# Performance work log

Measured on AMD Instinct MI355X. Metric: run time of the kernel, lower is better.

The kernel has to match this reference:

```python
import jax, jax.numpy as jnp
import numpy as np

LMAX = 6; MMAX = 2
C = 128          # num_channels
H = 8            # num_heads
ALPHA = 32       # attn_alpha_channels
VAL = 16         # attn_value_channels (H*VAL == C)
HID = 64         # attn_hidden_channels
FFN = 128        # ffn_hidden_channels
NL = 4           # num_layers
CUTOFF = 12.0; NRBF = 600
AVG_DEG = 23.395238876342773
AVG_NODES = 77.81317
EPS = 1e-16

def _maps():
    idx, ls = [], []
    for l in range(LMAX + 1):
        mm = min(l, MMAX)
        for m in range(-mm, mm + 1):
            idx.append(l * l + l + m); ls.append(l)
    return np.array(idx), np.array(ls)
_M2F_np, _LOF_np = _maps()
M2F = jnp.asarray(_M2F_np)   # [KM] full-coefficient index of each m-restricted coeff
LOF = jnp.asarray(_LOF_np)   # [KM] degree l of each m-restricted coeff
KM = int(_M2F_np.shape[0])   # 29 for lmax=6, mmax=2
KF = (LMAX + 1) ** 2         # 49

def _rbf(d):
    # GaussianSmearing(0, cutoff, NRBF, width_scalar=2.0)
    off = jnp.linspace(0.0, CUTOFF, NRBF)
    coeff = -0.5 / (2.0 * (off[1] - off[0])) ** 2
    return jnp.exp(coeff * (d[:, None] - off) ** 2)

def _envelope(d):
    # PolynomialEnvelope, exponent p=5
    x = d / CUTOFF
    env = 1.0 - 21.0 * x ** 5 + 35.0 * x ** 6 - 15.0 * x ** 7
    return jnp.where(x < 1.0, env, 0.0)

def _rms(x, g):
    # merge-norm over channel dim with learned per-channel scale
    return x * jax.lax.rsqrt(jnp.mean(x * x, axis=-1, keepdims=True) + 1e-6) * g

def _forward(atomic_numbers, edge_index, edge_distance, emb,
             We0, be0, We1, be1, Weproj, gamma1, gamma2,
             Wr0, Wr1, Wrl, Wmsg, Wap, wa, Wg, Wv, Wo,
             Wf1, Wfg, Wf2, Wh1, Wh2):
    N = atomic_numbers.shape[0]
    src, tgt = edge_index[0], edge_index[1]
    rbf = _rbf(edge_distance)            # [E, NRBF]
    env = _envelope(edge_distance)       # [E]
    # node init: atom embedding on the l=0 component
    x = jnp.zeros((N, KF, C), rbf.dtype).at[:, 0, :].set(emb[atomic_numbers])
    # edge-degree embedding: radial MLP -> per-edge coeffs -> scatter to targets
    h = jax.nn.silu(rbf @ We0 + be0)
    h = jax.nn.silu(h @ We1 + be1)
    deg = (h @ Weproj).reshape(-1, KM, C)              # [E, KM, C]
    x = x.at[tgt[:, None], M2F[None, :], :].add(deg / AVG_DEG)
    for i in range(NL):
        # ---- equivariant graph attention ----
        y = _rms(x, gamma1[i])
        ym = y[:, M2F, :]                               # [N, KM, C] m-restricted
        m = jnp.concatenate([ym[src], ym[tgt]], axis=-1)  # [E, KM, 2C]
        m = jnp.einsum('ekc,ch->ekh', m, Wmsg[i])       # [E, KM, HID]
        # radial function, shared across m within each l (use_rad_l_parametrization)
        rad = jax.nn.silu(jax.nn.silu(rbf @ Wr0[i]) @ Wr1[i])
        radl = rad @ Wrl[i]                             # [E, LMAX+1]
        m = m * radl[:, LOF][..., None]
        # attention logits from invariant (l=0) part
        a = jax.nn.silu(m[:, 0, :] @ Wap[i]).reshape(-1, H, ALPHA)
        logits = jnp.einsum('eha,ha->eh', a, wa[i])     # [E, H]
        segmax = jnp.full((N, H), -jnp.inf, logits.dtype).at[tgt].max(logits)
        ex = env[:, None] * jnp.exp(logits - segmax[tgt])  # envelope-masked softmax
        den = jax.ops.segment_sum(ex, tgt, num_segments=N)
        attn = ex / (den[tgt] + EPS)                    # [E, H]
        # SwiGLU-gated equivariant values
        g = jax.nn.silu(m[:, 0, :] @ Wg[i])             # [E, H*VAL]
        v = jnp.einsum('ekh,hv->ekv', m, Wv[i]) * g[:, None, :]
        v = v.reshape(-1, KM, H, VAL) * attn[:, None, :, None]
        agg = jax.ops.segment_sum(v.reshape(-1, KM, H * VAL), tgt, num_segments=N)
        out = jnp.einsum('nkv,vc->nkc', agg, Wo[i])     # [N, KM, C]
        x = x.at[:, M2F, :].add(out)
        # ---- feed-forward (grid-MLP style SwiGLU) ----
        y = _rms(x, gamma2[i])
        gf = jax.nn.silu(y[:, 0, :] @ Wfg[i])           # [N, FFN]
        hf = jnp.einsum('nkc,cf->nkf', y, Wf1[i]) * gf[:, None, :]
        x = x + jnp.einsum('nkf,fc->nkc', hf, Wf2[i])
    # energy head on invariant part, sum-aggregated over nodes
    s = jax.nn.silu(x[:, 0, :] @ Wh1) @ Wh2             # [N, 1]
    return (jnp.sum(s) / AVG_NODES).reshape(1)

def setup_inputs() -> dict:
    key = jax.random.key(0)
    ks = jax.random.split(key, 24)
    N, E = 6000, 120000
    def rn(k, shape, scale=0.05):
        return jax.random.normal(k, shape, dtype=jnp.float32) * scale
    inp = {}
    inp['atomic_numbers'] = jax.random.randint(ks[0], (N,), 0, 128)
    inp['edge_index'] = jax.random.randint(ks[1], (2, E), 0, N)
    inp['edge_distance'] = jax.random.uniform(ks[2], (E,), minval=0.5, maxval=CUTOFF, dtype=jnp.float32)
    inp['emb'] = rn(ks[3], (128, C), 1.0)
    inp['We0'] = rn(ks[4], (NRBF, 128)); inp['be0'] = jnp.zeros((128,), jnp.float32)
    inp['We1'] = rn(ks[5], (128, 128)); inp['be1'] = jnp.zeros((128,), jnp.float32)
    inp['Weproj'] = rn(ks[6], (128, KM * C))
    inp['gamma1'] = jnp.ones((NL, C), jnp.float32)
    inp['gamma2'] = jnp.ones((NL, C), jnp.float32)
    inp['Wr0'] = rn(ks[7], (NL, NRBF, 128))
    inp['Wr1'] = rn(ks[8], (NL, 128, 128))
    inp['Wrl'] = rn(ks[9], (NL, 128, LMAX + 1), 0.1)
    inp['Wmsg'] = rn(ks[10], (NL, 2 * C, HID))
    inp['Wap'] = rn(ks[11], (NL, HID, H * ALPHA))
    inp['wa'] = rn(ks[12], (NL, H, ALPHA))
    inp['Wg'] = rn(ks[13], (NL, HID, H * VAL))
    inp['Wv'] = rn(ks[14], (NL, HID, H * VAL))
    inp['Wo'] = rn(ks[15], (NL, H * VAL, C))
    inp['Wf1'] = rn(ks[16], (NL, C, FFN))
    inp['Wfg'] = rn(ks[17], (NL, C, FFN))
    inp['Wf2'] = rn(ks[18], (NL, FFN, C))
    inp['Wh1'] = rn(ks[19], (C, C))
    inp['Wh2'] = rn(ks[20], (C, 1))
    return inp

def reference(atomic_numbers, edge_index, edge_distance, emb,
              We0, be0, We1, be1, Weproj, gamma1, gamma2,
              Wr0, Wr1, Wrl, Wmsg, Wap, wa, Wg, Wv, Wo,
              Wf1, Wfg, Wf2, Wh1, Wh2):
    return _forward(atomic_numbers, edge_index, edge_distance, emb,
                    We0, be0, We1, be1, Weproj, gamma1, gamma2,
                    Wr0, Wr1, Wrl, Wmsg, Wap, wa, Wg, Wv, Wo,
                    Wf1, Wfg, Wf2, Wh1, Wh2)
```

## Files before the change

kernel.cpp:

```cpp
#include <hip/hip_runtime.h>

#define KM 29
#define GTAB 2048

typedef __bf16 bf16_t;
typedef __bf16 bf16x8 __attribute__((ext_vector_type(8)));
typedef __bf16 bf16x4 __attribute__((ext_vector_type(4)));
typedef __bf16 bf16x2 __attribute__((ext_vector_type(2)));
typedef float  f32x4  __attribute__((ext_vector_type(4)));
typedef float  f32x2  __attribute__((ext_vector_type(2)));

__device__ __forceinline__ float silu_f(float x){ return x / (1.0f + __expf(-x)); }

__device__ __forceinline__ float wave_reduce_sum(float v){
  #pragma unroll
  for (int s = 1; s < 64; s <<= 1) v += __shfl_xor(v, s);
  return v;
}

__device__ __forceinline__ constexpr int LOF2(int k){
  return (k<1)?0 : (k<4)?1 : (k<9)?2 : (k<14)?3 : (k<19)?4 : (k<24)?5 : 6;
}

__device__ __forceinline__ f32x4 mfma16(bf16x8 a, bf16x8 b, f32x4 c){
  return __builtin_amdgcn_mfma_f32_16x16x32_bf16(a, b, c, 0, 0, 0);
}

__device__ __forceinline__ float env_f(float d){
  float xx = d*(1.0f/12.0f);
  float x2 = xx*xx, x4 = x2*x2, x5 = x4*xx;
  float env = 1.0f - 21.0f*x5 + 35.0f*x5*xx - 15.0f*x5*x2;
  return (xx < 1.0f) ? env : 0.0f;
}

__global__ void k_count(const int* __restrict__ EI, int* __restrict__ cnt, int E){
  int e = blockIdx.x*256 + threadIdx.x;
  if (e < E) atomicAdd(&cnt[EI[E+e]], 1);
}

__global__ __launch_bounds__(1024) void k_scan(int* __restrict__ cnt, int* __restrict__ rowptr, int N){
  __shared__ int ts[1024];
  int t = threadIdx.x;
  int base = t*8;
  int loc[8]; int sum = 0;
  #pragma unroll
  for (int u = 0; u < 8; u++){ int idx = base+u; int v = (idx < N) ? cnt[idx] : 0; loc[u] = sum; sum += v; }
  ts[t] = sum; __syncthreads();
  for (int off = 1; off < 1024; off <<= 1){
    int v = (t >= off) ? ts[t-off] : 0;
    __syncthreads();
    ts[t] += v;
    __syncthreads();
  }
  int excl = ts[t] - sum;
  #pragma unroll
  for (int u = 0; u < 8; u++){
    int idx = base+u;
    if (idx < N){ int r = excl + loc[u]; rowptr[idx] = r; cnt[idx] = r; }
  }
  if (t == 1023) rowptr[N] = ts[1023];
}

__global__ void k_fill(const int* __restrict__ EI, int* __restrict__ cur, int* __restrict__ order, int E){
  int e = blockIdx.x*256 + threadIdx.x;
  if (e < E){ int pos = atomicAdd(&cur[EI[E+e]], 1); order[pos] = e; }
}

__global__ void k_sort(const int* __restrict__ rowptr, int* __restrict__ order, int N){
  int n = blockIdx.x*256 + threadIdx.x;
  if (n >= N) return;
  int rp = rowptr[n], re = rowptr[n+1];
  for (int a = rp+1; a < re; a++){
    int key = order[a]; int b = a-1;
    while (b >= rp && order[b] > key){ order[b+1] = order[b]; b--; }
    order[b+1] = key;
  }
}

__global__ void k_tr(const float* __restrict__ src, bf16_t* __restrict__ dst,
                     int L, int R, int C, int Lstr){
  int idx = blockIdx.x*256 + threadIdx.x;
  int total = L*R*C;
  if (idx >= total) return;
  int l = idx / (R*C); int rem = idx - l*(R*C);
  int r = rem / C; int c = rem - r*C;
  dst[((size_t)l*C + c)*R + r] = (bf16_t)src[(size_t)l*Lstr + (size_t)r*C + c];
}

__global__ void k_tr2(const float* __restrict__ src, bf16_t* __restrict__ dst){
  int idx = blockIdx.x*256 + threadIdx.x;
  if (idx >= 4*128*128) return;
  int l = idx >> 14; int j = (idx >> 7) & 127; int c = idx & 127;
  float v = (j < 64) ? src[(size_t)l*16384 + c*64 + j]
                     : src[(size_t)l*16384 + 8192 + c*64 + (j-64)];
  dst[idx] = (bf16_t)v;
}

__global__ __launch_bounds__(256) void k_tab_embed(
    const float* __restrict__ We0, const float* __restrict__ be0,
    const float* __restrict__ We1, const float* __restrict__ be1,
    const float* __restrict__ Wr0, const float* __restrict__ Wr1, const float* __restrict__ Wrl,
    float* __restrict__ h2tab, float* __restrict__ radtab)
{
  __shared__ float sb[4][640];
  const int wid = threadIdx.x >> 6, lane = threadIdx.x & 63;
  const int e = blockIdx.x*4 + wid;
  if (e >= GTAB) return;
  const float d = e * (12.0f/(GTAB-1));
  const float DLT = 12.0f/599.0f;
  const float CO  = -0.5f/((2.0f*DLT)*(2.0f*DLT));
  int jc = (int)(d/DLT + 0.5f);
  int j0 = jc - 16; if (j0 < 0) j0 = 0; if (j0 > 600-32) j0 = 600-32;
  float diff = d - (float)(j0+lane)*DLT;
  float gval = __expf(CO*diff*diff);
  float p[10];
  #pragma unroll
  for (int u = 0; u < 10; u++) p[u] = 0.f;
  const int c2 = 2*lane;
  for (int jj = 0; jj < 32; jj++){
    float gj = __shfl(gval, jj);
    int row = j0 + jj;
    const float2 w0 = *(const float2*)(We0 + row*128 + c2);
    p[0] += gj*w0.x; p[1] += gj*w0.y;
    #pragma unroll
    for (int i = 0; i < 4; i++){
      const float2 wr = *(const float2*)(Wr0 + ((size_t)i*600 + row)*128 + c2);
      p[2+2*i] += gj*wr.x; p[3+2*i] += gj*wr.y;
    }
  }
  sb[wid][c2]   = silu_f(p[0] + be0[c2]);
  sb[wid][c2+1] = silu_f(p[1] + be0[c2+1]);
  #pragma unroll
  for (int i = 0; i < 4; i++){
    sb[wid][128 + 128*i + c2]   = silu_f(p[2+2*i]);
    sb[wid][128 + 128*i + c2+1] = silu_f(p[3+2*i]);
  }
  float a0 = 0.f, a1 = 0.f;
  for (int c = 0; c < 128; c++){
    float hv = sb[wid][c];
    const float2 w = *(const float2*)(We1 + c*128 + c2);
    a0 += hv*w.x; a1 += hv*w.y;
  }
  a0 = silu_f(a0 + be1[c2]); a1 = silu_f(a1 + be1[c2+1]);
  h2tab[(size_t)e*128 + c2]     = a0;
  h2tab[(size_t)e*128 + c2 + 1] = a1;
  #pragma unroll
  for (int i = 0; i < 4; i++){
    float r0 = 0.f, r1 = 0.f;
    const float* W1 = Wr1 + (size_t)i*128*128;
    for (int c = 0; c < 128; c++){
      float rv = sb[wid][128 + 128*i + c];
      const float2 w = *(const float2*)(W1 + c*128 + c2);
      r0 += rv*w.x; r1 += rv*w.y;
    }
    r0 = silu_f(r0); r1 = silu_f(r1);
    const float* Wl = Wrl + (size_t)i*128*7;
    float pl[7];
    #pragma unroll
    for (int l = 0; l < 7; l++) pl[l] = r0*Wl[c2*7+l] + r1*Wl[(c2+1)*7+l];
    #pragma unroll
// ... 232 lines not shown
    #pragma unroll
    for (int r = 0; r < 4; r++){
      int e = eb + lg*4 + r;
      if (e < E) gate16[(size_t)e*128 + col] = (bf16_t)silu_f(accG[u][r]);
    }
  }
  #pragma unroll
  for (int hpair = 0; hpair < 2; hpair++){
    int c0 = 64*wid + hpair*32 + l15;
    float w0 = wav[c0], w1 = wav[c0+16];
    float s[4];
    #pragma unroll
    for (int r = 0; r < 4; r++)
      s[r] = silu_f(accA[2*hpair][r])*w0 + silu_f(accA[2*hpair+1][r])*w1;
    #pragma unroll
    for (int r = 0; r < 4; r++){
      s[r] += __shfl_xor(s[r], 1);
      s[r] += __shfl_xor(s[r], 2);
      s[r] += __shfl_xor(s[r], 4);
      s[r] += __shfl_xor(s[r], 8);
    }
    if (l15 == 0){
      #pragma unroll
      for (int r = 0; r < 4; r++){
        int e = eb + lg*4 + r;
        if (e < E) expat[(size_t)e*8 + 2*wid + hpair] = envs[lg*4 + r] * __expf(s[r]);
      }
    }
  }
}

#define FMA_DW(dw, kb) { \
  f32x2 lo_ = __builtin_amdgcn_cvt_pk_f32_fp8((dw), false); \
  f32x2 hi_ = __builtin_amdgcn_cvt_pk_f32_fp8((dw), true); \
  acc[(kb)]   += lo_.x * rw[LOF2((kb))]; \
  acc[(kb)+1] += lo_.y * rw[LOF2((kb)+1)]; \
  acc[(kb)+2] += hi_.x * rw[LOF2((kb)+2)]; \
  acc[(kb)+3] += hi_.y * rw[LOF2((kb)+3)]; }

__global__ __launch_bounds__(512, 4) void k_gather(
    const int* __restrict__ EI, const int* __restrict__ rowptr, const int* __restrict__ order,
    const unsigned char* __restrict__ PV8, const unsigned char* __restrict__ QV8,
    const bf16_t* __restrict__ gate16, const float* __restrict__ expat,
    const float* __restrict__ radl,
    bf16_t* __restrict__ agg)
{
  __shared__ bf16_t mA[32*136];
  __shared__ bf16_t mB[32*136];
  __shared__ float at8[512];
  __shared__ float rl7[512];
  __shared__ int   esb[64], srcs[64];
  __shared__ float denl[32];

  int n = blockIdx.x, t = threadIdx.x;
  int rp = rowptr[n], deg = rowptr[n+1] - rp;
  if (deg == 0){
    for (int idx = t; idx < 3712; idx += 512) agg[(size_t)n*3712 + idx] = (bf16_t)0.f;
    return;
  }
  int eg = t >> 7, hv = t & 127, h = hv >> 4;
  float acc[32];
  #pragma unroll
  for (int j = 0; j < 32; j++) acc[j] = 0.f;
  float S[7];
  #pragma unroll
  for (int l = 0; l < 7; l++) S[l] = 0.f;
  float dpart = 0.f;
  for (int base = 0; base < deg; base += 64){
    int ne = min(64, deg - base);
    if (base > 0) __syncthreads();
    if (t < ne){ int e = order[rp + base + t]; esb[t] = e; srcs[t] = EI[e]; }
    __syncthreads();
    if (t < ne*8){
      int i = t >> 3, q = t & 7;
      int e = esb[i];
      at8[t] = expat[(size_t)e*8 + q];
      if (q < 7) rl7[t] = radl[(size_t)e*7 + q];
    }
    __syncthreads();
    uint4 A0 = {0,0,0,0}, A1 = {0,0,0,0}, B0 = {0,0,0,0}, B1 = {0,0,0,0};
    float gA = 0.f, gB = 0.f;
    int i = eg;
    if (i < ne){
      const uint4* p = (const uint4*)(PV8 + (size_t)srcs[i]*4096 + hv*32);
      A0 = p[0]; A1 = p[1];
      gA = (float)gate16[(size_t)esb[i]*128 + hv];
    }
    if (i + 4 < ne){
      const uint4* p = (const uint4*)(PV8 + (size_t)srcs[i+4]*4096 + hv*32);
      B0 = p[0]; B1 = p[1];
      gB = (float)gate16[(size_t)esb[i+4]*128 + hv];
    }
    while (i < ne){
      int i2 = i + 8;
      uint4 C0 = {0,0,0,0}, C1 = {0,0,0,0}; float gC = 0.f;
      if (i2 < ne){
        const uint4* p = (const uint4*)(PV8 + (size_t)srcs[i2]*4096 + hv*32);
        C0 = p[0]; C1 = p[1];
        gC = (float)gate16[(size_t)esb[i2]*128 + hv];
      }
      float ae = at8[i*8 + h];
      dpart += ae;
      float w = gA * ae;
      float rw[7];
      #pragma unroll
      for (int l = 0; l < 7; l++){ rw[l] = rl7[i*8 + l]*w; S[l] += rw[l]; }
      FMA_DW(A0.x, 0)  FMA_DW(A0.y, 4)  FMA_DW(A0.z, 8)  FMA_DW(A0.w, 12)
      FMA_DW(A1.x, 16) FMA_DW(A1.y, 20) FMA_DW(A1.z, 24) FMA_DW(A1.w, 28)
      A0 = B0; A1 = B1; gA = gB;
      B0 = C0; B1 = C1; gB = gC;
      i += 4;
    }
  }
  {
    const unsigned char* qvp = QV8 + (size_t)n*4096 + hv*32;
    uint4 q0 = *(const uint4*)qvp;
    uint4 q1 = *(const uint4*)(qvp + 16);
    float rw[7];
    #pragma unroll
    for (int l = 0; l < 7; l++) rw[l] = S[l];
    FMA_DW(q0.x, 0)  FMA_DW(q0.y, 4)  FMA_DW(q0.z, 8)  FMA_DW(q0.w, 12)
    FMA_DW(q1.x, 16) FMA_DW(q1.y, 20) FMA_DW(q1.z, 24) FMA_DW(q1.w, 28)
  }
  if ((hv & 15) == 0) denl[eg*8 + h] = dpart;
  __syncthreads();
  {
    float dsum = denl[h] + denl[8 + h] + denl[16 + h] + denl[24 + h];
    float inv = 1.0f/(dsum + 1e-30f);
    #pragma unroll
    for (int j = 0; j < 32; j++) acc[j] *= inv;
  }
  if (eg == 0){
    #pragma unroll
    for (int j = 0; j < 32; j++) mA[j*136 + hv] = (bf16_t)acc[j];
  } else if (eg == 1){
    #pragma unroll
    for (int j = 0; j < 32; j++) mB[j*136 + hv] = (bf16_t)acc[j];
  }
  __syncthreads();
  if (eg == 2){
    #pragma unroll
    for (int j = 0; j < 32; j++) mA[j*136 + hv] = (bf16_t)((float)mA[j*136 + hv] + acc[j]);
  } else if (eg == 3){
    #pragma unroll
    for (int j = 0; j < 32; j++) mB[j*136 + hv] = (bf16_t)((float)mB[j*136 + hv] + acc[j]);
  }
  __syncthreads();
  for (int idx = t; idx < 3712; idx += 512){
    int k = idx >> 7, c = idx & 127;
    agg[(size_t)n*3712 + idx] = (bf16_t)((float)mA[k*136 + c] + (float)mB[k*136 + c]);
  }
}

__global__ __launch_bounds__(512, 4) void k_xupdate(
    const bf16_t* __restrict__ agg,
    const float* __restrict__ gamma1, const float* __restrict__ gamma2,
    const float* __restrict__ Wfg,
    const bf16_t* __restrict__ Wf1T, const bf16_t* __restrict__ Wf2T,
    const bf16_t* __restrict__ WoT, const bf16_t* __restrict__ WmsgCT, const bf16_t* __restrict__ WvT,
    bf16_t* __restrict__ Xb, int layer,
    unsigned char* __restrict__ PV8o, unsigned char* __restrict__ QV8o,
    float* __restrict__ P0o, float* __restrict__ Q0o, int do_tail, int N)
{
  __shared__ float  xs[3712];
  __shared__ bf16_t ysag[32*136];
  __shared__ bf16_t hsqv[32*136];
  __shared__ float  pf[640];

  int n = blockIdx.x, t = threadIdx.x;
  int wid = t >> 6, lane = t & 63;

  {
    const bf16x2* Xp2 = (const bf16x2*)(Xb + (size_t)n*3712);
    for (int p = t; p < 1856; p += 512){
      bf16x2 v = Xp2[p];
      xs[2*p]   = (float)v.x;
      xs[2*p+1] = (float)v.y;
    }
  }
  for (int idx = t; idx < 3712; idx += 512){
    int k = idx >> 7, c = idx & 127;
    ysag[k*136 + c] = agg[(size_t)n*3712 + idx];
  }
  for (int idx = t; idx < 3*136; idx += 512) ysag[29*136 + idx] = (bf16_t)0.f;
  __syncthreads();
  {
    const bf16_t* Bt = WoT + (size_t)layer*16384;
    int mtile = wid >> 2, colt = (wid & 3)*2;
    int row = mtile*16 + (lane & 15);
    int koff = (lane >> 4)*8;
    f32x4 a2[2] = {{0,0,0,0},{0,0,0,0}};
    #pragma unroll
    for (int kk = 0; kk < 128; kk += 32){
      bf16x8 a = *(const bf16x8*)(ysag + row*136 + kk + koff);
      #pragma unroll
      for (int u = 0; u < 2; u++){
        int col = (colt+u)*16 + (lane & 15);
        bf16x8 b = *(const bf16x8*)(Bt + (size_t)col*128 + kk + koff);
        a2[u] = mfma16(a, b, a2[u]);
      }
    }
    #pragma unroll
    for (int u = 0; u < 2; u++){
      int col = (colt+u)*16 + (lane & 15);
      #pragma unroll
      for (int r = 0; r < 4; r++){
        int r32 = mtile*16 + (lane>>4)*4 + r;
        if (r32 < KM) xs[r32*128 + col] += a2[u][r];
      }
    }
  }
  __syncthreads();
  {
    const float* g2 = gamma2 + layer*128;
    for (int k = wid; k < KM; k += 8){
      float x0 = xs[k*128 + lane], x1 = xs[k*128 + 64 + lane];
      float ss = wave_reduce_sum(x0*x0 + x1*x1);
      float sc = rsqrtf(ss*(1.0f/128.0f) + 1e-6f);
      ysag[k*136 + lane]      = (bf16_t)(x0*sc*g2[lane]);
      ysag[k*136 + 64 + lane] = (bf16_t)(x1*sc*g2[64+lane]);
    }
    for (int idx = t; idx < 3*136; idx += 512) ysag[29*136 + idx] = (bf16_t)0.f;
  }
  __syncthreads();
  {
    int part = t >> 7, f = t & 127;
    const float* Wfgp = Wfg + (size_t)layer*16384;
    float p = 0.f;
    for (int c = part*32; c < part*32 + 32; c++) p += (float)ysag[c] * Wfgp[c*128 + f];
    pf[part*128 + f] = p;
  }
  __syncthreads();
  if (t < 128) pf[512 + t] = silu_f(pf[t] + pf[128+t] + pf[256+t] + pf[384+t]);
  __syncthreads();
  {
    const bf16_t* Bt = Wf1T + (size_t)layer*16384;
    int mtile = wid >> 2, colt = (wid & 3)*2;
    int row = mtile*16 + (lane & 15);
    int koff = (lane >> 4)*8;
    f32x4 a2[2] = {{0,0,0,0},{0,0,0,0}};
    #pragma unroll
    for (int kk = 0; kk < 128; kk += 32){
      bf16x8 a = *(const bf16x8*)(ysag + row*136 + kk + koff);
      #pragma unroll
      for (int u = 0; u < 2; u++){
        int col = (colt+u)*16 + (lane & 15);
        bf16x8 b = *(const bf16x8*)(Bt + (size_t)col*128 + kk + koff);
        a2[u] = mfma16(a, b, a2[u]);
      }
    }
    #pragma unroll
    for (int u = 0; u < 2; u++){
      int col = (colt+u)*16 + (lane & 15);
      float gfc = pf[512 + col];
      #pragma unroll
      for (int r = 0; r < 4; r++){
        int r32 = mtile*16 + (lane>>4)*4 + r;
        hsqv[r32*136 + col] = (bf16_t)(a2[u][r]*gfc);
      }
    }
  }
  __syncthreads();
  {
    const bf16_t* Bt = Wf2T + (size_t)layer*16384;
    int mtile = wid >> 2, colt = (wid & 3)*2;
    int row = mtile*16 + (lane & 15);
    int koff = (lane >> 4)*8;
    f32x4 a2[2] = {{0,0,0,0},{0,0,0,0}};
    #pragma unroll
    for (int kk = 0; kk < 128; kk += 32){
      bf16x8 a = *(const bf16x8*)(hsqv + row*136 + kk + koff);
      #pragma unroll
      for (int u = 0; u < 2; u++){
        int col = (colt+u)*16 + (lane & 15);
        bf16x8 b = *(const bf16x8*)(Bt + (size_t)col*128 + kk + koff);
        a2[u] = mfma16(a, b, a2[u]);
      }
    }
    #pragma unroll
    for (int u = 0; u < 2; u++){
      int col = (colt+u)*16 + (lane & 15);
      #pragma unroll
      for (int r = 0; r < 4; r++){
        int r32 = mtile*16 + (lane>>4)*4 + r;
        if (r32 < KM) xs[r32*128 + col] += a2[u][r];
      }
    }
  }
  __syncthreads();
  {
    bf16x2* Xp2 = (bf16x2*)(Xb + (size_t)n*3712);
    for (int p = t; p < 1856; p += 512){
      bf16x2 v;
      v.x = (bf16_t)xs[2*p];
      v.y = (bf16_t)xs[2*p+1];
      Xp2[p] = v;
    }
  }
  if (!do_tail) return;
  {
    const float* g1n = gamma1 + (size_t)(layer+1)*128;
    for (int k = wid; k < KM; k += 8){
      float x0 = xs[k*128 + lane], x1 = xs[k*128 + 64 + lane];
      float ss = wave_reduce_sum(x0*x0 + x1*x1);
      float sc = rsqrtf(ss*(1.0f/128.0f) + 1e-6f);
      ysag[k*136 + lane]      = (bf16_t)(x0*sc*g1n[lane]);
      ysag[k*136 + 64 + lane] = (bf16_t)(x1*sc*g1n[64+lane]);
    }
  }
  __syncthreads();
  {
    int mtile = wid >> 2;
    int row = mtile*16 + (lane & 15);
    int koff = (lane >> 4)*8;
    {
      const bf16_t* Bc = WmsgCT + (size_t)(layer+1)*16384;
      f32x4 acc[2] = {{0,0,0,0},{0,0,0,0}};
      #pragma unroll
      for (int kk = 0; kk < 128; kk += 32){
        bf16x8 a = *(const bf16x8*)(ysag + row*136 + kk + koff);
        #pragma unroll
        for (int u = 0; u < 2; u++){
          int col = ((wid&3)*2+u)*16 + (lane & 15);
          bf16x8 b = *(const bf16x8*)(Bc + (size_t)col*128 + kk + koff);
          acc[u] = mfma16(a, b, acc[u]);
        }
      }
      #pragma unroll
      for (int u = 0; u < 2; u++){
        int col = ((wid&3)*2+u)*16 + (lane & 15);
        #pragma unroll
        for (int r = 0; r < 4; r++){
          int r32 = mtile*16 + (lane>>4)*4 + r;
          hsqv[r32*136 + col] = (bf16_t)acc[u][r];
        }
        if (mtile == 0 && ((lane>>4) == 0)){
          float v = acc[u][0];
          if (col < 64) P0o[(size_t)n*64 + col] = v;
          else          Q0o[(size_t)n*64 + col - 64] = v;
        }
      }
    }
    __syncthreads();
    {
      const bf16_t* Bt = WvT + (size_t)(layer+1)*8192;
      f32x4 accP[2] = {{0,0,0,0},{0,0,0,0}};
      f32x4 accQ[2] = {{0,0,0,0},{0,0,0,0}};
      #pragma unroll
      for (int kk = 0; kk < 64; kk += 32){
        bf16x8 aP = *(const bf16x8*)(hsqv + row*136 + kk + koff);
        bf16x8 aQ = *(const bf16x8*)(hsqv + row*136 + 64 + kk + koff);
        #pragma unroll
        for (int u = 0; u < 2; u++){
          int col = ((wid&3)*2+u)*16 + (lane & 15);
          bf16x8 b = *(const bf16x8*)(Bt + (size_t)col*64 + kk + koff);
          accP[u] = mfma16(aP, b, accP[u]);
          accQ[u] = mfma16(aQ, b, accQ[u]);
        }
      }
      unsigned char* pvp = PV8o + (size_t)n*4096;
      unsigned char* qvp = QV8o + (size_t)n*4096;
      int r0i = mtile*16 + (lane>>4)*4;
      #pragma unroll
      for (int u = 0; u < 2; u++){
        int col = ((wid&3)*2+u)*16 + (lane & 15);
        float pk[4], qk[4];
        #pragma unroll
        for (int r = 0; r < 4; r++){
          int r32 = r0i + r;
          pk[r] = (r32 < KM) ? accP[u][r] : 0.f;
          qk[r] = (r32 < KM) ? accQ[u][r] : 0.f;
        }
        int dw = __builtin_amdgcn_cvt_pk_fp8_f32(pk[0], pk[1], 0, false);
        dw = __builtin_amdgcn_cvt_pk_fp8_f32(pk[2], pk[3], dw, true);
        *(unsigned int*)(pvp + col*32 + r0i) = (unsigned int)dw;
        int dw2 = __builtin_amdgcn_cvt_pk_fp8_f32(qk[0], qk[1], 0, false);
        dw2 = __builtin_amdgcn_cvt_pk_fp8_f32(qk[2], qk[3], dw2, true);
        *(unsigned int*)(qvp + col*32 + r0i) = (unsigned int)dw2;
      }
    }
  }
}

__global__ __launch_bounds__(256) void k_head(
    const bf16_t* __restrict__ Xb, const float* __restrict__ Wh1, const float* __restrict__ Wh2,
    float* __restrict__ partial, int N)
{
  __shared__ float wsum[4];
  int t = threadIdx.x;
  int half = t >> 7;
  int n = blockIdx.x*2 + half;
  int f = t & 127;
  float sv = 0.f;
  if (n < N){
    const bf16_t* xp = Xb + (size_t)n*3712;
    float acc = 0.f;
    for (int c = 0; c < 128; c++) acc += (float)xp[c]*Wh1[c*128 + f];
    sv = silu_f(acc)*Wh2[f];
  }
  sv = wave_reduce_sum(sv);
  if ((t & 63) == 0) wsum[t >> 6] = sv;
  __syncthreads();
  if (t == 0) partial[blockIdx.x] = wsum[0] + wsum[1] + wsum[2] + wsum[3];
}

__global__ __launch_bounds__(256) void k_reduce(const float* __restrict__ partial, float* __restrict__ out, int P){
  __shared__ float sh[256];
  int t = threadIdx.x;
  float s = 0.f;
  for (int i = t; i < P; i += 256) s += partial[i];
  sh[t] = s; __syncthreads();
  for (int off = 128; off > 0; off >>= 1){
    if (t < off) sh[t] += sh[t+off];
    __syncthreads();
  }
  if (t == 0) out[0] = sh[0] / 77.81317f;
}

extern "C" void kernel_launch(void* const* d_in, const int* in_sizes, int n_in,
                              void* d_out, int out_size, void* d_ws, size_t ws_size,
                              hipStream_t stream)
{
  const int*   Z      = (const int*)d_in[0];
  const int*   EI     = (const int*)d_in[1];
  const float* ed     = (const float*)d_in[2];
  const float* emb    = (const float*)d_in[3];
  const float* We0    = (const float*)d_in[4];
  const float* be0    = (const float*)d_in[5];
  const float* We1    = (const float*)d_in[6];
  const float* be1    = (const float*)d_in[7];
  const float* Weproj = (const float*)d_in[8];
  const float* gamma1 = (const float*)d_in[9];
  const float* gamma2 = (const float*)d_in[10];
  const float* Wr0    = (const float*)d_in[11];
  const float* Wr1    = (const float*)d_in[12];
  const float* Wrl    = (const float*)d_in[13];
  const float* Wmsg   = (const float*)d_in[14];
  const float* Wap    = (const float*)d_in[15];
  const float* wa     = (const float*)d_in[16];
  const float* Wg     = (const float*)d_in[17];
  const float* Wv     = (const float*)d_in[18];
  const float* Wo     = (const float*)d_in[19];
  const float* Wf1    = (const float*)d_in[20];
  const float* Wfg    = (const float*)d_in[21];
  const float* Wf2    = (const float*)d_in[22];
  const float* Wh1    = (const float*)d_in[23];
  const float* Wh2    = (const float*)d_in[24];

  const int N = in_sizes[0];
  const int E = in_sizes[2];

  float* ws = (float*)d_ws;
  size_t o = 0;
  auto alloc = [&](size_t nf){ float* p = ws + o; o += (nf + 7) & ~(size_t)7; return p; };

  bf16_t* Xb    = (bf16_t*)alloc((size_t)N*1856);
  float* P0     = alloc((size_t)N*64);
  float* Q0     = alloc((size_t)N*64);
  float* expat  = alloc((size_t)E*8);
  float* radl   = alloc((size_t)E*7);
  float* part   = alloc((size_t)((N+1)/2) + 8);
  float* radtab = alloc((size_t)GTAB*28);
  float* h2tab  = alloc((size_t)GTAB*128);
  bf16_t* h2sum = (bf16_t*)alloc((size_t)N*64);
  unsigned char* PV8 = (unsigned char*)alloc((size_t)N*1024);
  unsigned char* QV8 = (unsigned char*)alloc((size_t)N*1024);
  bf16_t* agg   = (bf16_t*)alloc((size_t)N*1856);
  bf16_t* gate16= (bf16_t*)alloc((size_t)E*64);
  bf16_t* arena = (bf16_t*)alloc(434176);
  int* rowptr = (int*)alloc((size_t)N+8);
  int* curs   = (int*)alloc((size_t)N);
  int* order  = (int*)alloc((size_t)E);

  bf16_t* WmsgCT  = arena;
  bf16_t* WvT     = arena + 65536;
  bf16_t* WoT     = arena + 98304;
  bf16_t* Wf1T    = arena + 163840;
  bf16_t* Wf2T    = arena + 229376;
  bf16_t* WapT    = arena + 294912;
  bf16_t* WgT     = arena + 360448;
  bf16_t* WeprojT = arena + 393216;

  hipMemsetAsync(curs, 0, sizeof(int)*N, stream);
  k_count<<<(E+255)/256, 256, 0, stream>>>(EI, curs, E);
  k_scan<<<1, 1024, 0, stream>>>(curs, rowptr, N);
  k_fill<<<(E+255)/256, 256, 0, stream>>>(EI, curs, order, E);
  k_sort<<<(N+255)/256, 256, 0, stream>>>(rowptr, order, N);

  k_tr2<<<256, 256, 0, stream>>>(Wmsg, WmsgCT);
  k_tr<<<128, 256, 0, stream>>>(Wv,   WvT,  4, 64, 128, 8192);
  k_tr<<<256, 256, 0, stream>>>(Wo,   WoT,  4, 128, 128, 16384);
  k_tr<<<256, 256, 0, stream>>>(Wf1,  Wf1T, 4, 128, 128, 16384);
  k_tr<<<256, 256, 0, stream>>>(Wf2,  Wf2T, 4, 128, 128, 16384);
  k_tr<<<256, 256, 0, stream>>>(Wap,  WapT, 4, 64, 256, 16384);
  k_tr<<<128, 256, 0, stream>>>(Wg,   WgT,  4, 64, 128, 8192);
  k_tr<<<1856, 256, 0, stream>>>(Weproj, WeprojT, 1, 128, 3712, 0);

  k_tab_embed<<<GTAB/4, 256, 0, stream>>>(We0, be0, We1, be1, Wr0, Wr1, Wrl, h2tab, radtab);
  k_h2sum<<<(N+1)/2, 256, 0, stream>>>(ed, h2tab, rowptr, order, h2sum, N);
  k_init_x<<<(N+31)/32, 256, 0, stream>>>(Z, emb, WeprojT, h2sum, Xb, N);

  k_pqv<<<N, 512, 0, stream>>>(Xb, gamma1, WmsgCT, WvT, PV8, QV8, P0, Q0, 0);

  for (int i = 0; i < 4; i++){
    k_edge_logits<<<(E+15)/16, 256, 0, stream>>>(EI, ed, P0, Q0, radtab, WapT, wa, WgT,
                                                 expat, radl, gate16, E, i);
    k_gather<<<N, 512, 0, stream>>>(EI, rowptr, order, PV8, QV8, gate16, expat, radl, agg);
    k_xupdate<<<N, 512, 0, stream>>>(agg, gamma1, gamma2, Wfg, Wf1T, Wf2T, WoT, WmsgCT, WvT,
                                     Xb, i, PV8, QV8, P0, Q0, (i < 3) ? 1 : 0, N);
  }

  int PB = (N+1)/2;
  k_head<<<PB, 256, 0, stream>>>(Xb, Wh1, Wh2, part, N);
  k_reduce<<<1, 256, 0, stream>>>(part, (float*)d_out, PB);
}
```

Before: 2.049 ms.

## Split per-node xupdate into four multi-node MFMA kernels with register-held weights reuse

Replaces the single per-node k_xupdate kernel (one 512-thread block per node) with four kernels: Wo, Wf1, Wf2 and next-layer P/Q/V projection. Each processes 4 nodes per 256-thread block, so each wave computes a 32x128 tile and reuses each weight fragment across two M-tiles. Intermediates are round-tripped through global buffers (agg reused, new gfb for the gate). The residual stream is now kept in bf16 between steps instead of fp32 in shared memory. The intent is better MFMA utilisation and weight reuse, at the cost of extra launches, extra global traffic and slightly lower precision of intermediate sums.

```diff
diff --git a/kernel.cpp b/kernel.cpp
--- a/kernel.cpp
+++ b/kernel.cpp
@@ -5,7 +5,6 @@
 
 typedef __bf16 bf16_t;
 typedef __bf16 bf16x8 __attribute__((ext_vector_type(8)));
-typedef __bf16 bf16x4 __attribute__((ext_vector_type(4)));
 typedef __bf16 bf16x2 __attribute__((ext_vector_type(2)));
 typedef float  f32x4  __attribute__((ext_vector_type(4)));
 typedef float  f32x2  __attribute__((ext_vector_type(2)));
@@ -544,231 +543,355 @@
   }
 }
 
-__global__ __launch_bounds__(512, 4) void k_xupdate(
-    const bf16_t* __restrict__ agg,
-    const float* __restrict__ gamma1, const float* __restrict__ gamma2,
-    const float* __restrict__ Wfg,
-    const bf16_t* __restrict__ Wf1T, const bf16_t* __restrict__ Wf2T,
-    const bf16_t* __restrict__ WoT, const bf16_t* __restrict__ WmsgCT, const bf16_t* __restrict__ WvT,
-    bf16_t* __restrict__ Xb, int layer,
-    unsigned char* __restrict__ PV8o, unsigned char* __restrict__ QV8o,
-    float* __restrict__ P0o, float* __restrict__ Q0o, int do_tail, int N)
-{
-  __shared__ float  xs[3712];
-  __shared__ bf16_t ysag[32*136];
-  __shared__ bf16_t hsqv[32*136];
-  __shared__ float  pf[640];
-
-  int n = blockIdx.x, t = threadIdx.x;
-  int wid = t >> 6, lane = t & 63;
-
-  {
-    const bf16x2* Xp2 = (const bf16x2*)(Xb + (size_t)n*3712);
-    for (int p = t; p < 1856; p += 512){
-      bf16x2 v = Xp2[p];
-      xs[2*p]   = (float)v.x;
-      xs[2*p+1] = (float)v.y;
-    }
-  }
-  for (int idx = t; idx < 3712; idx += 512){
-    int k = idx >> 7, c = idx & 127;
-    ysag[k*136 + c] = agg[(size_t)n*3712 + idx];
-  }
-  for (int idx = t; idx < 3*136; idx += 512) ysag[29*136 + idx] = (bf16_t)0.f;
-  __syncthreads();
-  {
-    const bf16_t* Bt = WoT + (size_t)layer*16384;
-    int mtile = wid >> 2, colt = (wid & 3)*2;
-    int row = mtile*16 + (lane & 15);
-    int koff = (lane >> 4)*8;
-    f32x4 a2[2] = {{0,0,0,0},{0,0,0,0}};
-    #pragma unroll
-    for (int kk = 0; kk < 128; kk += 32){
-      bf16x8 a = *(const bf16x8*)(ysag + row*136 + kk + koff);
-      #pragma unroll
-      for (int u = 0; u < 2; u++){
-        int col = (colt+u)*16 + (lane & 15);
-        bf16x8 b = *(const bf16x8*)(Bt + (size_t)col*128 + kk + koff);
-        a2[u] = mfma16(a, b, a2[u]);
-      }
-    }
-    #pragma unroll
-    for (int u = 0; u < 2; u++){
-      int col = (colt+u)*16 + (lane & 15);
+
+__device__ __forceinline__ void flat_load(const bf16_t* __restrict__ src, bf16_t* aLDS,
+                                          int n0, int N, int t){
+  for (int p = t; p < 4*1856; p += 256){
+    int node = p / 1856, rem = p - node*1856;
+    int k = rem >> 6, cp = rem & 63;
+    bf16x2 v; v.x = (bf16_t)0.f; v.y = (bf16_t)0.f;
+    if (n0 + node < N) v = *(const bf16x2*)(src + (size_t)(n0+node)*3712 + k*128 + cp*2);
+    *(bf16x2*)(aLDS + (node*32 + k)*136 + cp*2) = v;
+  }
+  for (int p = t; p < 4*3*136; p += 256){
+    int node = p / 408, rem = p - node*408;
+    aLDS[(node*32 + 29)*136 + rem] = (bf16_t)0.f;
+  }
+}
+
+__global__ __launch_bounds__(256, 4) void k_wo(
+    bf16_t* __restrict__ agg,
+    const bf16_t* __restrict__ WoT, bf16_t* __restrict__ Xb,
+    const float* __restrict__ gamma2, const float* __restrict__ Wfg,
+    float* __restrict__ gfb, int layer, int N)
+{
+  __shared__ bf16_t aLDS[128*136];
+  __shared__ bf16_t y0[4*128];
+  int t = threadIdx.x, wid = t >> 6, lane = t & 63;
+  int l15 = lane & 15, lg = lane >> 4, koff = lg*8;
+  int n0 = blockIdx.x*4;
+
+  flat_load(agg, aLDS, n0, N, t);
+  __syncthreads();
+  bf16x8 af[2][4];
+  #pragma unroll
+  for (int m = 0; m < 2; m++)
+    #pragma unroll
+    for (int kc = 0; kc < 4; kc++)
+      af[m][kc] = *(const bf16x8*)(aLDS + (wid*32 + m*16 + l15)*136 + kc*32 + koff);
+  __syncthreads();
+  flat_load(Xb, aLDS, n0, N, t);
+  f32x4 C[2][8];
+  #pragma unroll
+  for (int m = 0; m < 2; m++)
+    #pragma unroll
+    for (int u = 0; u < 8; u++) C[m][u] = (f32x4){0,0,0,0};
+  const bf16_t* Bt = WoT + (size_t)layer*16384;
+  #pragma unroll
+  for (int kc = 0; kc < 4; kc++){
+    #pragma unroll
+    for (int u = 0; u < 8; u++){
+      int col = u*16 + l15;
+      bf16x8 b = *(const bf16x8*)(Bt + (size_t)col*128 + kc*32 + koff);
+      C[0][u] = mfma16(af[0][kc], b, C[0][u]);
+      C[1][u] = mfma16(af[1][kc], b, C[1][u]);
+    }
+  }
+  __syncthreads();
+  #pragma unroll
+  for (int m = 0; m < 2; m++)
+    #pragma unroll
+    for (int u = 0; u < 8; u++){
+      int col = u*16 + l15;
       #pragma unroll
       for (int r = 0; r < 4; r++){
-        int r32 = mtile*16 + (lane>>4)*4 + r;
-        if (r32 < KM) xs[r32*128 + col] += a2[u][r];
-      }
-    }
-  }
-  __syncthreads();
-  {
-    const float* g2 = gamma2 + layer*128;
-    for (int k = wid; k < KM; k += 8){
-      float x0 = xs[k*128 + lane], x1 = xs[k*128 + 64 + lane];
+        int row = wid*32 + m*16 + lg*4 + r;
+        float xn = (float)aLDS[row*136 + col] + C[m][u][r];
+        aLDS[row*136 + col] = (bf16_t)xn;
+      }
+    }
+  __syncthreads();
+  const float* g2 = gamma2 + layer*128;
+  for (int r32 = wid; r32 < 128; r32 += 4){
+    int node = r32 >> 5, k = r32 & 31;
+    if (k >= KM || n0 + node >= N) continue;
+    float x0 = (float)aLDS[r32*136 + lane], x1 = (float)aLDS[r32*136 + 64 + lane];
+    float ss = wave_reduce_sum(x0*x0 + x1*x1);
+    float sc = rsqrtf(ss*(1.0f/128.0f) + 1e-6f);
+    bf16_t yv0 = (bf16_t)(x0*sc*g2[lane]), yv1 = (bf16_t)(x1*sc*g2[64+lane]);
+    size_t gb = (size_t)(n0+node)*3712 + k*128;
+    Xb[gb + lane] = (bf16_t)x0; Xb[gb + 64 + lane] = (bf16_t)x1;
+    agg[gb + lane] = yv0; agg[gb + 64 + lane] = yv1;
+    if (k == 0){ y0[node*128 + lane] = yv0; y0[node*128 + 64 + lane] = yv1; }
+  }
+  __syncthreads();
+  const float* Wfgp = Wfg + (size_t)layer*16384;
+  for (int p = t; p < 512; p += 256){
+    int node = p >> 7, f = p & 127;
+    if (n0 + node < N){
+      float g = 0.f;
+      for (int c = 0; c < 128; c++) g += (float)y0[node*128 + c]*Wfgp[c*128 + f];
+      gfb[(size_t)(n0+node)*128 + f] = silu_f(g);
+    }
+  }
+}
+
+__global__ __launch_bounds__(256, 4) void k_wf1(
+    bf16_t* __restrict__ ysb,
+    const float* __restrict__ gfb, const bf16_t* __restrict__ Wf1T, int layer, int N)
+{
+  __shared__ bf16_t aLDS[128*136];
+  __shared__ float gfs[4*128];
+  int t = threadIdx.x, wid = t >> 6, lane = t & 63;
+  int l15 = lane & 15, lg = lane >> 4, koff = lg*8;
+  int n0 = blockIdx.x*4;
+
+  flat_load(ysb, aLDS, n0, N, t);
+  for (int p = t; p < 512; p += 256){
+    int node = p >> 7, f = p & 127;
+    gfs[p] = (n0 + node < N) ? gfb[(size_t)(n0+node)*128 + f] : 0.f;
+  }
+  __syncthreads();
+  bf16x8 af[2][4];
+  #pragma unroll
+  for (int m = 0; m < 2; m++)
+    #pragma unroll
+    for (int kc = 0; kc < 4; kc++)
+      af[m][kc] = *(const bf16x8*)(aLDS + (wid*32 + m*16 + l15)*136 + kc*32 + koff);
+  f32x4 C[2][8];
+  #pragma unroll
+  for (int m = 0; m < 2; m++)
+    #pragma unroll
+    for (int u = 0; u < 8; u++) C[m][u] = (f32x4){0,0,0,0};
+  const bf16_t* Bt = Wf1T + (size_t)layer*16384;
+  #pragma unroll
+  for (int kc = 0; kc < 4; kc++){
+    #pragma unroll
+    for (int u = 0; u < 8; u++){
+      int col = u*16 + l15;
+      bf16x8 b = *(const bf16x8*)(Bt + (size_t)col*128 + kc*32 + koff);
+      C[0][u] = mfma16(af[0][kc], b, C[0][u]);
+      C[1][u] = mfma16(af[1][kc], b, C[1][u]);
+    }
+  }
+  #pragma unroll
+  for (int m = 0; m < 2; m++)
+    #pragma unroll
+    for (int u = 0; u < 8; u++){
+      int col = u*16 + l15;
+      float gfc = gfs[wid*128 + col];
+      #pragma unroll
+      for (int r = 0; r < 4; r++){
+        int row = wid*32 + m*16 + lg*4 + r;
+        aLDS[row*136 + col] = (bf16_t)(C[m][u][r]*gfc);
+      }
+    }
+  __syncthreads();
+  for (int p = t; p < 4*1856; p += 256){
+    int node = p / 1856, rem = p - node*1856;
+    int k = rem >> 6, cp = rem & 63;
+    if (n0 + node < N)
+      *(bf16x2*)(ysb + (size_t)(n0+node)*3712 + k*128 + cp*2) =
+          *(const bf16x2*)(aLDS + (node*32 + k)*136 + cp*2);
+  }
+}
+
+__global__ __launch_bounds__(256, 4) void k_wf2(
+    bf16_t* __restrict__ hsb,
+    const bf16_t* __restrict__ Wf2T, bf16_t* __restrict__ Xb,
+    const float* __restrict__ gamma1, int layerNext, int do_ys1, int N)
+{
+  __shared__ bf16_t aLDS[128*136];
+  int t = threadIdx.x, wid = t >> 6, lane = t & 63;
+  int l15 = lane & 15, lg = lane >> 4, koff = lg*8;
+  int n0 = blockIdx.x*4;
+
+  flat_load(hsb, aLDS, n0, N, t);
+  __syncthreads();
+  bf16x8 af[2][4];
+  #pragma unroll
+  for (int m = 0; m < 2; m++)
+    #pragma unroll
+    for (int kc = 0; kc < 4; kc++)
+      af[m][kc] = *(const bf16x8*)(aLDS + (wid*32 + m*16 + l15)*136 + kc*32 + koff);
+  __syncthreads();
+  flat_load(Xb, aLDS, n0, N, t);
+  f32x4 C[2][8];
+  #pragma unroll
+  for (int m = 0; m < 2; m++)
+    #pragma unroll
+    for (int u = 0; u < 8; u++) C[m][u] = (f32x4){0,0,0,0};
+  const bf16_t* Bt = Wf2T + (size_t)layerNext*16384 - 16384;
+  #pragma unroll
+  for (int kc = 0; kc < 4; kc++){
+    #pragma unroll
+    for (int u = 0; u < 8; u++){
+      int col = u*16 + l15;
+      bf16x8 b = *(const bf16x8*)(Bt + (size_t)col*128 + kc*32 + koff);
+      C[0][u] = mfma16(af[0][kc], b, C[0][u]);
+      C[1][u] = mfma16(af[1][kc], b, C[1][u]);
+    }
+  }
+  __syncthreads();
+  #pragma unroll
+  for (int m = 0; m < 2; m++)
+    #pragma unroll
+    for (int u = 0; u < 8; u++){
+      int col = u*16 + l15;
+      #pragma unroll
+      for (int r = 0; r < 4; r++){
+        int row = wid*32 + m*16 + lg*4 + r;
+        float xn = (float)aLDS[row*136 + col] + C[m][u][r];
+        aLDS[row*136 + col] = (bf16_t)xn;
+      }
+    }
+  __syncthreads();
+  const float* g1 = gamma1 + (size_t)layerNext*128;
+  for (int r32 = wid; r32 < 128; r32 += 4){
+    int node = r32 >> 5, k = r32 & 31;
+    if (k >= KM || n0 + node >= N) continue;
+    float x0 = (float)aLDS[r32*136 + lane], x1 = (float)aLDS[r32*136 + 64 + lane];
+    size_t gb = (size_t)(n0+node)*3712 + k*128;
+    Xb[gb + lane] = (bf16_t)x0; Xb[gb + 64 + lane] = (bf16_t)x1;
+    if (do_ys1){
       float ss = wave_reduce_sum(x0*x0 + x1*x1);
       float sc = rsqrtf(ss*(1.0f/128.0f) + 1e-6f);
-      ysag[k*136 + lane]      = (bf16_t)(x0*sc*g2[lane]);
-      ysag[k*136 + 64 + lane] = (bf16_t)(x1*sc*g2[64+lane]);
-    }
-    for (int idx = t; idx < 3*136; idx += 512) ysag[29*136 + idx] = (bf16_t)0.f;
-  }
-  __syncthreads();
+      hsb[gb + lane]      = (bf16_t)(x0*sc*g1[lane]);
+      hsb[gb + 64 + lane] = (bf16_t)(x1*sc*g1[64+lane]);
+    }
+  }
+}
+
+__global__ __launch_bounds__(256, 4) void k_pqnext(
+    const bf16_t* __restrict__ ysb,
+    const bf16_t* __restrict__ WmsgCT, const bf16_t* __restrict__ WvT,
+    unsigned char* __restrict__ PV8, unsigned char* __restrict__ QV8,
+    float* __restrict__ P0, float* __restrict__ Q0, int layerNext, int N)
+{
+  __shared__ bf16_t aLDS[128*136];
+  int t = threadIdx.x, wid = t >> 6, lane = t & 63;
+  int l15 = lane & 15, lg = lane >> 4, koff = lg*8;
+  int n0 = blockIdx.x*4;
+
+  flat_load(ysb, aLDS, n0, N, t);
+  __syncthreads();
+  bf16x8 af[2][4];
+  #pragma unroll
+  for (int m = 0; m < 2; m++)
+    #pragma unroll
+    for (int kc = 0; kc < 4; kc++)
+      af[m][kc] = *(const bf16x8*)(aLDS + (wid*32 + m*16 + l15)*136 + kc*32 + koff);
+  f32x4 C[2][8];
+  #pragma unroll
+  for (int m = 0; m < 2; m++)
+    #pragma unroll
+    for (int u = 0; u < 8; u++) C[m][u] = (f32x4){0,0,0,0};
+  const bf16_t* Bc = WmsgCT + (size_t)layerNext*16384;
+  #pragma unroll
+  for (int kc = 0; kc < 4; kc++){
+    #pragma unroll
+    for (int u = 0; u < 8; u++){
+      int col = u*16 + l15;
+      bf16x8 b = *(const bf16x8*)(Bc + (size_t)col*128 + kc*32 + koff);
+      C[0][u] = mfma16(af[0][kc], b, C[0][u]);
+      C[1][u] = mfma16(af[1][kc], b, C[1][u]);
+    }
+  }
+  #pragma unroll
+  for (int m = 0; m < 2; m++)
+    #pragma unroll
+    for (int u = 0; u < 8; u++){
+      int col = u*16 + l15;
+      #pragma unroll
+      for (int r = 0; r < 4; r++){
+        int row = wid*32 + m*16 + lg*4 + r;
+        aLDS[row*136 + col] = (bf16_t)C[m][u][r];
+      }
+      if (m == 0 && lg == 0 && n0 + wid < N){
+        float v = C[0][u][0];
+        if (col < 64) P0[(size_t)(n0+wid)*64 + col] = v;
+        else          Q0[(size_t)(n0+wid)*64 + col - 64] = v;
+      }
+    }
+  __syncthreads();
+  const bf16_t* Bt = WvT + (size_t)layerNext*8192;
   {
-    int part = t >> 7, f = t & 127;
-    const float* Wfgp = Wfg + (size_t)layer*16384;
-    float p = 0.f;
-    for (int c = part*32; c < part*32 + 32; c++) p += (float)ysag[c] * Wfgp[c*128 + f];
-    pf[part*128 + f] = p;
-  }
-  __syncthreads();
-  if (t < 128) pf[512 + t] = silu_f(pf[t] + pf[128+t] + pf[256+t] + pf[384+t]);
-  __syncthreads();
+    bf16x8 ap[2][2];
+    #pragma unroll
+    for (int m = 0; m < 2; m++)
+      #pragma unroll
+      for (int kc = 0; kc < 2; kc++)
+        ap[m][kc] = *(const bf16x8*)(aLDS + (wid*32 + m*16 + l15)*136 + kc*32 + koff);
+    f32x4 P[2][8];
+    #pragma unroll
+    for (int m = 0; m < 2; m++)
+      #pragma unroll
+      for (int u = 0; u < 8; u++) P[m][u] = (f32x4){0,0,0,0};
+    #pragma unroll
+    for (int kc = 0; kc < 2; kc++){
+      #pragma unroll
+      for (int u = 0; u < 8; u++){
+        int col = u*16 + l15;
+        bf16x8 b = *(const bf16x8*)(Bt + (size_t)col*64 + kc*32 + koff);
+        P[0][u] = mfma16(ap[0][kc], b, P[0][u]);
+        P[1][u] = mfma16(ap[1][kc], b, P[1][u]);
+      }
+    }
+    if (n0 + wid < N){
+      unsigned char* pvp = PV8 + (size_t)(n0+wid)*4096;
+      #pragma unroll
+      for (int m = 0; m < 2; m++){
+        int k0 = m*16 + lg*4;
+        #pragma unroll
+        for (int u = 0; u < 8; u++){
+          int col = u*16 + l15;
+          float pk[4];
+          #pragma unroll
+          for (int r = 0; r < 4; r++) pk[r] = (k0 + r < KM) ? P[m][u][r] : 0.f;
+          int dw = __builtin_amdgcn_cvt_pk_fp8_f32(pk[0], pk[1], 0, false);
+          dw = __builtin_amdgcn_cvt_pk_fp8_f32(pk[2], pk[3], dw, true);
+          *(unsigned int*)(pvp + col*32 + k0) = (unsigned int)dw;
+        }
+      }
+    }
+  }
   {
-    const bf16_t* Bt = Wf1T + (size_t)layer*16384;
-    int mtile = wid >> 2, colt = (wid & 3)*2;
-    int row = mtile*16 + (lane & 15);
-    int koff = (lane >> 4)*8;
-    f32x4 a2[2] = {{0,0,0,0},{0,0,0,0}};
-    #pragma unroll
-    for (int kk = 0; kk < 128; kk += 32){
-      bf16x8 a = *(const bf16x8*)(ysag + row*136 + kk + koff);
-      #pragma unroll
-      for (int u = 0; u < 2; u++){
-        int col = (colt+u)*16 + (lane & 15);
-        bf16x8 b = *(const bf16x8*)(Bt + (size_t)col*128 + kk + koff);
-        a2[u] = mfma16(a, b, a2[u]);
-      }
-    }
-    #pragma unroll
-    for (int u = 0; u < 2; u++){
-      int col = (colt+u)*16 + (lane & 15);
-      float gfc = pf[512 + col];
-      #pragma unroll
-      for (int r = 0; r < 4; r++){
-        int r32 = mtile*16 + (lane>>4)*4 + r;
-        hsqv[r32*136 + col] = (bf16_t)(a2[u][r]*gfc);
-      }
-    }
-  }
-  __syncthreads();
-  {
-    const bf16_t* Bt = Wf2T + (size_t)layer*16384;
-    int mtile = wid >> 2, colt = (wid & 3)*2;
-    int row = mtile*16 + (lane & 15);
-    int koff = (lane >> 4)*8;
-    f32x4 a2[2] = {{0,0,0,0},{0,0,0,0}};
-    #pragma unroll
-    for (int kk = 0; kk < 128; kk += 32){
-      bf16x8 a = *(const bf16x8*)(hsqv + row*136 + kk + koff);
-      #pragma unroll
-      for (int u = 0; u < 2; u++){
-        int col = (colt+u)*16 + (lane & 15);
-        bf16x8 b = *(const bf16x8*)(Bt + (size_t)col*128 + kk + koff);
-        a2[u] = mfma16(a, b, a2[u]);
-      }
-    }
-    #pragma unroll
-    for (int u = 0; u < 2; u++){
-      int col = (colt+u)*16 + (lane & 15);
-      #pragma unroll
-      for (int r = 0; r < 4; r++){
-        int r32 = mtile*16 + (lane>>4)*4 + r;
-        if (r32 < KM) xs[r32*128 + col] += a2[u][r];
-      }
-    }
-  }
-  __syncthreads();
-  {
-    bf16x2* Xp2 = (bf16x2*)(Xb + (size_t)n*3712);
-    for (int p = t; p < 1856; p += 512){
-      bf16x2 v;
-      v.x = (bf16_t)xs[2*p];
-      v.y = (bf16_t)xs[2*p+1];
-      Xp2[p] = v;
-    }
-  }
-  if (!do_tail) return;
-  {
-    const float* g1n = gamma1 + (size_t)(layer+1)*128;
-    for (int k = wid; k < KM; k += 8){
-      float x0 = xs[k*128 + lane], x1 = xs[k*128 + 64 + lane];
-      float ss = wave_reduce_sum(x0*x0 + x1*x1);
-      float sc = rsqrtf(ss*(1.0f/128.0f) + 1e-6f);
-      ysag[k*136 + lane]      = (bf16_t)(x0*sc*g1n[lane]);
-      ysag[k*136 + 64 + lane] = (bf16_t)(x1*sc*g1n[64+lane]);
-    }
-  }
-  __syncthreads();
-  {
-    int mtile = wid >> 2;
-    int row = mtile*16 + (lane & 15);
-    int koff = (lane >> 4)*8;
-    {
-      const bf16_t* Bc = WmsgCT + (size_t)(layer+1)*16384;
-      f32x4 acc[2] = {{0,0,0,0},{0,0,0,0}};
-      #pragma unroll
-      for (int kk = 0; kk < 128; kk += 32){
-        bf16x8 a = *(const bf16x8*)(ysag + row*136 + kk + koff);
+    bf16x8 aq[2][2];
+    #pragma unroll
+    for (int m = 0; m < 2; m++)
+      #pragma unroll
+      for (int kc = 0; kc < 2; kc++)
+        aq[m][kc] = *(const bf16x8*)(aLDS + (wid*32 + m*16 + l15)*136 + 64 + kc*32 + koff);
+    f32x4 Qc[2][8];
+    #pragma unroll
+    for (int m = 0; m < 2; m++)
+      #pragma unroll
+      for (int u = 0; u < 8; u++) Qc[m][u] = (f32x4){0,0,0,0};
+    #pragma unroll
+    for (int kc = 0; kc < 2; kc++){
+      #pragma unroll
+      for (int u = 0; u < 8; u++){
+        int col = u*16 + l15;
+        bf16x8 b = *(const bf16x8*)(Bt + (size_t)col*64 + kc*32 + koff);
+        Qc[0][u] = mfma16(aq[0][kc], b, Qc[0][u]);
+        Qc[1][u] = mfma16(aq[1][kc], b, Qc[1][u]);
+      }
+    }
+    if (n0 + wid < N){
+      unsigned char* qvp = QV8 + (size_t)(n0+wid)*4096;
+      #pragma unroll
+      for (int m = 0; m < 2; m++){
+        int k0 = m*16 + lg*4;
         #pragma unroll
-        for (int u = 0; u < 2; u++){
-          int col = ((wid&3)*2+u)*16 + (lane & 15);
-          bf16x8 b = *(const bf16x8*)(Bc + (size_t)col*128 + kk + koff);
-          acc[u] = mfma16(a, b, acc[u]);
+        for (int u = 0; u < 8; u++){
+          int col = u*16 + l15;
+          float qk[4];
+          #pragma unroll
+          for (int r = 0; r < 4; r++) qk[r] = (k0 + r < KM) ? Qc[m][u][r] : 0.f;
+          int dw2 = __builtin_amdgcn_cvt_pk_fp8_f32(qk[0], qk[1], 0, false);
+          dw2 = __builtin_amdgcn_cvt_pk_fp8_f32(qk[2], qk[3], dw2, true);
+          *(unsigned int*)(qvp + col*32 + k0) = (unsigned int)dw2;
         }
-      }
-      #pragma unroll
-      for (int u = 0; u < 2; u++){
-        int col = ((wid&3)*2+u)*16 + (lane & 15);
-        #pragma unroll
-        for (int r = 0; r < 4; r++){
-          int r32 = mtile*16 + (lane>>4)*4 + r;
-          hsqv[r32*136 + col] = (bf16_t)acc[u][r];
-        }
-        if (mtile == 0 && ((lane>>4) == 0)){
-          float v = acc[u][0];
-          if (col < 64) P0o[(size_t)n*64 + col] = v;
-          else          Q0o[(size_t)n*64 + col - 64] = v;
-        }
-      }
-    }
-    __syncthreads();
-    {
-      const bf16_t* Bt = WvT + (size_t)(layer+1)*8192;
-      f32x4 accP[2] = {{0,0,0,0},{0,0,0,0}};
-      f32x4 accQ[2] = {{0,0,0,0},{0,0,0,0}};
-      #pragma unroll
-      for (int kk = 0; kk < 64; kk += 32){
-        bf16x8 aP = *(const bf16x8*)(hsqv + row*136 + kk + koff);
-        bf16x8 aQ = *(const bf16x8*)(hsqv + row*136 + 64 + kk + koff);
-        #pragma unroll
-        for (int u = 0; u < 2; u++){
-          int col = ((wid&3)*2+u)*16 + (lane & 15);
-          bf16x8 b = *(const bf16x8*)(Bt + (size_t)col*64 + kk + koff);
-          accP[u] = mfma16(aP, b, accP[u]);
-          accQ[u] = mfma16(aQ, b, accQ[u]);
-        }
-      }
-      unsigned char* pvp = PV8o + (size_t)n*4096;
-      unsigned char* qvp = QV8o + (size_t)n*4096;
-      int r0i = mtile*16 + (lane>>4)*4;
-      #pragma unroll
-      for (int u = 0; u < 2; u++){
-        int col = ((wid&3)*2+u)*16 + (lane & 15);
-        float pk[4], qk[4];
-        #pragma unroll
-        for (int r = 0; r < 4; r++){
-          int r32 = r0i + r;
-          pk[r] = (r32 < KM) ? accP[u][r] : 0.f;
-          qk[r] = (r32 < KM) ? accQ[u][r] : 0.f;
-        }
-        int dw = __builtin_amdgcn_cvt_pk_fp8_f32(pk[0], pk[1], 0, false);
-        dw = __builtin_amdgcn_cvt_pk_fp8_f32(pk[2], pk[3], dw, true);
-        *(unsigned int*)(pvp + col*32 + r0i) = (unsigned int)dw;
-        int dw2 = __builtin_amdgcn_cvt_pk_fp8_f32(qk[0], qk[1], 0, false);
-        dw2 = __builtin_amdgcn_cvt_pk_fp8_f32(qk[2], qk[3], dw2, true);
-        *(unsigned int*)(qvp + col*32 + r0i) = (unsigned int)dw2;
       }
     }
   }
@@ -855,6 +978,7 @@
   float* radtab = alloc((size_t)GTAB*28);
   float* h2tab  = alloc((size_t)GTAB*128);
   bf16_t* h2sum = (bf16_t*)alloc((size_t)N*64);
+  float* gfb    = alloc((size_t)N*128);
   unsigned char* PV8 = (unsigned char*)alloc((size_t)N*1024);
   unsigned char* QV8 = (unsigned char*)alloc((size_t)N*1024);
   bf16_t* agg   = (bf16_t*)alloc((size_t)N*1856);
@@ -894,12 +1018,16 @@
 
   k_pqv<<<N, 512, 0, stream>>>(Xb, gamma1, WmsgCT, WvT, PV8, QV8, P0, Q0, 0);
 
+  const int FB = (N + 3)/4;
   for (int i = 0; i < 4; i++){
     k_edge_logits<<<(E+15)/16, 256, 0, stream>>>(EI, ed, P0, Q0, radtab, WapT, wa, WgT,
                                                  expat, radl, gate16, E, i);
     k_gather<<<N, 512, 0, stream>>>(EI, rowptr, order, PV8, QV8, gate16, expat, radl, agg);
-    k_xupdate<<<N, 512, 0, stream>>>(agg, gamma1, gamma2, Wfg, Wf1T, Wf2T, WoT, WmsgCT, WvT,
-                                     Xb, i, PV8, QV8, P0, Q0, (i < 3) ? 1 : 0, N);
+    k_wo  <<<FB, 256, 0, stream>>>(agg, WoT, Xb, gamma2, Wfg, gfb, i, N);
+    k_wf1 <<<FB, 256, 0, stream>>>(agg, gfb, Wf1T, i, N);
+    k_wf2 <<<FB, 256, 0, stream>>>(agg, Wf2T, Xb, gamma1, i+1, (i < 3) ? 1 : 0, N);
+    if (i < 3)
+      k_pqnext<<<FB, 256, 0, stream>>>(agg, WmsgCT, WvT, PV8, QV8, P0, Q0, i+1, N);
   }
 
   int PB = (N+1)/2;
```

New measurement: 2.338 ms. 1.14x slower.
